# Kernel tuning notes

Hardware: AMD Instinct MI355X
Metric: run time of the kernel (lower is better)

## Reference

```python
import jax, jax.numpy as jnp
import numpy as np

# Ramamoorthi-Hanrahan irradiance matrix constants
C1d, C2d, C3d, C4d, C5d = 0.429043, 0.511664, 0.743125, 0.886227, 0.247708
# Real SH evaluation constants (degree 0..4), standard plenoxels/3DGS values
_SH_C0 = 0.28209479177387814
_SH_C1 = 0.4886025119029199
_SH_C2 = np.array([1.0925484305920792, -1.0925484305920792, 0.31539156525252005, -1.0925484305920792, 0.5462742152960396], np.float32)
_SH_C3 = np.array([-0.5900435899266435, 2.890611442640554, -0.4570457994644658, 0.3731763325901154, -0.4570457994644658, 1.445305721320277, -0.5900435899266435], np.float32)
_SH_C4 = np.array([2.5033429417967046, -1.7701307697799304, 0.9461746957575601, -0.6690465435572892, 0.10578554691520431, -0.6690465435572892, 0.47308734787878004, -1.7701307697799304, 0.6258357354491761], np.float32)
_L = np.array([l for l in range(5) for _ in range(2 * l + 1)], np.float32)  # SH band index per coeff (25,)
_MI = np.array([0, 0, 0, 0, 1, 1, 1, 2, 2, 3])  # triu_indices(4,4)
_MJ = np.array([0, 1, 2, 3, 1, 2, 3, 2, 3, 3])


def safe_normalize(x, eps=1e-20):
    return x * jax.lax.rsqrt(jnp.maximum(jnp.sum(x * x, -1, keepdims=True), eps))


def sh_basis(d):
    # d: (N,3) directions -> (N,25) real SH basis up to degree 4
    x, y, z = d[..., 0], d[..., 1], d[..., 2]
    xx, yy, zz = x * x, y * y, z * z
    xy, yz, xz = x * y, y * z, x * z
    b = [jnp.full_like(x, _SH_C0),
         -_SH_C1 * y, _SH_C1 * z, -_SH_C1 * x,
         _SH_C2[0] * xy, _SH_C2[1] * yz, _SH_C2[2] * (2.0 * zz - xx - yy), _SH_C2[3] * xz, _SH_C2[4] * (xx - yy),
         _SH_C3[0] * y * (3.0 * xx - yy), _SH_C3[1] * xy * z, _SH_C3[2] * y * (4.0 * zz - xx - yy),
         _SH_C3[3] * z * (2.0 * zz - 3.0 * xx - 3.0 * yy), _SH_C3[4] * x * (4.0 * zz - xx - yy),
         _SH_C3[5] * z * (xx - yy), _SH_C3[6] * x * (xx - 3.0 * yy),
         _SH_C4[0] * xy * (xx - yy), _SH_C4[1] * yz * (3.0 * xx - yy), _SH_C4[2] * xy * (7.0 * zz - 1.0),
         _SH_C4[3] * yz * (7.0 * zz - 3.0), _SH_C4[4] * (zz * (35.0 * zz - 30.0) + 3.0),
         _SH_C4[5] * xz * (7.0 * zz - 3.0), _SH_C4[6] * (xx - yy) * (7.0 * zz - 1.0),
         _SH_C4[7] * xz * (xx - yy), _SH_C4[8] * (xx * (xx - 3.0 * yy) - yy * (3.0 * xx - yy))]
    return jnp.stack(b, -1)


def bilinear_lut(lut, uv):
    # lut: (H,W,2); uv: (N,2) in [0,1]; linear filter, clamp boundary (nvdiffrast texel-center convention)
    H, W, _ = lut.shape
    x = uv[:, 0] * W - 0.5
    y = uv[:, 1] * H - 0.5
    x0 = jnp.floor(x); y0 = jnp.floor(y)
    fx = (x - x0)[:, None]; fy = (y - y0)[:, None]
    x0i = jnp.clip(x0.astype(jnp.int32), 0, W - 1); x1i = jnp.clip(x0i + 1, 0, W - 1)
    y0i = jnp.clip(y0.astype(jnp.int32), 0, H - 1); y1i = jnp.clip(y0i + 1, 0, H - 1)
    v00 = lut[y0i, x0i]; v01 = lut[y0i, x1i]; v10 = lut[y1i, x0i]; v11 = lut[y1i, x1i]
    return (v00 * (1.0 - fx) + v01 * fx) * (1.0 - fy) + (v10 * (1.0 - fx) + v11 * fx) * fy


def shade(gb_pos, gb_normal, albedo, ks, kr, km, view_pos, base, fg_lut):
    wo = safe_normalize(view_pos - gb_pos)
    n = gb_normal
    reflvec = safe_normalize(2.0 * jnp.sum(wo * n, -1, keepdims=True) * n - wo)
    # --- diffuse irradiance: n_h^T M n_h per color channel (RH quadratic form) ---
    n_h = jnp.concatenate([n, jnp.ones_like(n[:, :1])], -1)  # (N,4)
    e = base  # (25,3)
    triu = jnp.stack([C1d * e[8], C1d * e[4], C1d * e[7], C2d * e[3], -C1d * e[8],
                      C1d * e[5], C2d * e[1], C3d * e[6], C2d * e[2], C4d * e[0] - C5d * e[6]], 0)  # (10,3)
    M = jnp.zeros((4, 4, 3), base.dtype).at[_MI, _MJ].set(triu).at[_MJ, _MI].set(triu)  # symmetric (4,4,3)
    diffuse_irr = jnp.einsum('ni,ijc,nj->nc', n_h, M, n_h)  # (N,3)
    diffuse = albedo * diffuse_irr
    # --- specular ---
    NdotV = jnp.maximum(jnp.sum(wo * n, -1, keepdims=True), 1e-4)
    fg = bilinear_lut(fg_lut, jnp.concatenate([NdotV, kr], -1))  # (N,2)
    gwk = jnp.exp(-(_L * (_L + 1.0))[None, :] * (kr * kr))  # (N,25) Gauss-Weierstrass kernel per SH band
    spec_irr = gwk[:, :, None] * base[None]  # (N,25,3)
    spec_rad = jnp.einsum('nk,nkc->nc', sh_basis(reflvec), spec_irr)  # (N,3)
    F0 = (1.0 - km) * 0.04 + albedo * km
    reflectance = F0 * fg[:, :1] + fg[:, 1:2]
    spec = spec_rad * reflectance
    rgb = jax.nn.sigmoid(diffuse + spec)
    return rgb, diffuse, spec


def setup_inputs() -> dict:
    key = jax.random.key(0)
    k = jax.random.split(key, 9)
    N = 1048576  # 1024x1024 pixels
    return {
        'gb_pos': jax.random.normal(k[0], (N, 3), jnp.float32),
        'gb_normal': jax.random.normal(k[1], (N, 3), jnp.float32),
        'albedo': jax.random.uniform(k[2], (N, 3), jnp.float32),
        'ks': jax.random.uniform(k[3], (N, 1), jnp.float32),
        'kr': jax.random.uniform(k[4], (N, 1), jnp.float32),
        'km': jax.random.uniform(k[5], (N, 1), jnp.float32),
        'view_pos': jax.random.normal(k[6], (N, 3), jnp.float32),
        'base': jax.random.normal(k[7], (25, 3), jnp.float32) * 0.5,
        'fg_lut': jax.random.uniform(k[8], (256, 256, 2), jnp.float32),
    }


def reference(gb_pos, gb_normal, albedo, ks, kr, km, view_pos, base, fg_lut):
    return shade(gb_pos, gb_normal, albedo, ks, kr, km, view_pos, base, fg_lut)
```

## Files before the change

### kernel.cpp

```cpp
#include <hip/hip_runtime.h>
#include <math.h>


__device__ __forceinline__ void shade_pixel(
    float px, float py, float pz,
    float nx, float ny, float nz,
    float ax, float ay, float az,
    float krv, float kmv,
    float vx, float vy, float vz,
    const float* __restrict__ eb, const float* __restrict__ fg_lut,
    float* rgb, float* dif, float* spc)
{
    float wx = vx - px, wy = vy - py, wz = vz - pz;
    float wl2 = wx*wx + wy*wy + wz*wz;
    float winv = __builtin_amdgcn_rsqf(fmaxf(wl2, 1e-20f));
    wx *= winv; wy *= winv; wz *= winv;

    float ndv = wx*nx + wy*ny + wz*nz;

    float rx = 2.0f*ndv*nx - wx;
    float ry = 2.0f*ndv*ny - wy;
    float rz = 2.0f*ndv*nz - wz;
    float rl2 = rx*rx + ry*ry + rz*rz;
    float rinv = __builtin_amdgcn_rsqf(fmaxf(rl2, 1e-20f));
    rx *= rinv; ry *= rinv; rz *= rinv;

    float NdotV = fmaxf(ndv, 1e-4f);
    float xf = NdotV * 256.0f - 0.5f;
    float yf = krv   * 256.0f - 0.5f;
    float x0f = floorf(xf), y0f = floorf(yf);
    float fx = xf - x0f, fy = yf - y0f;
    int x0i = min(max((int)x0f, 0), 255);
    int x1i = min(x0i + 1, 255);
    int y0i = min(max((int)y0f, 0), 255);
    int y1i = min(y0i + 1, 255);
    const float2* lut2 = (const float2*)fg_lut;
    float2 t00 = lut2[(y0i << 8) + x0i];
    float2 t01 = lut2[(y0i << 8) + x1i];
    float2 t10 = lut2[(y1i << 8) + x0i];
    float2 t11 = lut2[(y1i << 8) + x1i];
    float gxw = 1.0f - fx, gyw = 1.0f - fy;
    float fg0 = (t00.x*gxw + t01.x*fx)*gyw + (t10.x*gxw + t11.x*fx)*fy;
    float fg1 = (t00.y*gxw + t01.y*fx)*gyw + (t10.y*gxw + t11.y*fx)*fy;

    float k2 = krv*krv;
    float g1 = __expf( -2.0f*k2);
    float g2 = __expf( -6.0f*k2);
    float g3 = __expf(-12.0f*k2);
    float g4 = __expf(-20.0f*k2);

    float xx = rx*rx, yy = ry*ry, zz = rz*rz;
    float xy = rx*ry, yz = ry*rz, xz = rx*rz;

    float sr0 = 0.0f, sr1 = 0.0f, sr2 = 0.0f;
#define SHACC(K, EXPR) do { float bk_ = (EXPR);                      \
        sr0 = fmaf(bk_, eb[3*(K)+0], sr0);                           \
        sr1 = fmaf(bk_, eb[3*(K)+1], sr1);                           \
        sr2 = fmaf(bk_, eb[3*(K)+2], sr2); } while (0)

    SHACC(0,  0.28209479177387814f);
    SHACC(1,  (-0.4886025119029199f*ry) * g1);
    SHACC(2,  ( 0.4886025119029199f*rz) * g1);
    SHACC(3,  (-0.4886025119029199f*rx) * g1);
    SHACC(4,  ( 1.0925484305920792f*xy) * g2);
    SHACC(5,  (-1.0925484305920792f*yz) * g2);
    SHACC(6,  ( 0.31539156525252005f*(2.0f*zz - xx - yy)) * g2);
    SHACC(7,  (-1.0925484305920792f*xz) * g2);
    SHACC(8,  ( 0.5462742152960396f*(xx - yy)) * g2);
    SHACC(9,  (-0.5900435899266435f*ry*(3.0f*xx - yy)) * g3);
    SHACC(10, ( 2.890611442640554f*xy*rz) * g3);
    SHACC(11, (-0.4570457994644658f*ry*(4.0f*zz - xx - yy)) * g3);
    SHACC(12, ( 0.3731763325901154f*rz*(2.0f*zz - 3.0f*xx - 3.0f*yy)) * g3);
    SHACC(13, (-0.4570457994644658f*rx*(4.0f*zz - xx - yy)) * g3);
    SHACC(14, ( 1.445305721320277f*rz*(xx - yy)) * g3);
    SHACC(15, (-0.5900435899266435f*rx*(xx - 3.0f*yy)) * g3);
    SHACC(16, ( 2.5033429417967046f*xy*(xx - yy)) * g4);
    SHACC(17, (-1.7701307697799304f*yz*(3.0f*xx - yy)) * g4);
    SHACC(18, ( 0.9461746957575601f*xy*(7.0f*zz - 1.0f)) * g4);
    SHACC(19, (-0.6690465435572892f*yz*(7.0f*zz - 3.0f)) * g4);
    SHACC(20, ( 0.10578554691520431f*(zz*(35.0f*zz - 30.0f) + 3.0f)) * g4);
    SHACC(21, (-0.6690465435572892f*xz*(7.0f*zz - 3.0f)) * g4);
    SHACC(22, ( 0.47308734787878004f*(xx - yy)*(7.0f*zz - 1.0f)) * g4);
    SHACC(23, (-1.7701307697799304f*xz*(xx - yy)) * g4);
    SHACC(24, ( 0.6258357354491761f*(xx*(xx - 3.0f*yy) - yy*(3.0f*xx - yy))) * g4);
#undef SHACC

    float q0  = nx*nx - ny*ny;
    float qz  = nz*nz;
    float qxy = nx*ny, qxz = nx*nz, qyz = ny*nz;

    float alb[3] = {ax, ay, az};
    float srs[3] = {sr0, sr1, sr2};
    #pragma unroll
    for (int c = 0; c < 3; ++c) {
        float e0 = eb[0*3+c], e1 = eb[1*3+c], e2 = eb[2*3+c], e3 = eb[3*3+c],
              e4 = eb[4*3+c], e5 = eb[5*3+c], e6 = eb[6*3+c], e7 = eb[7*3+c],
              e8 = eb[8*3+c];
        float irr = 0.429043f*e8*q0 + 0.743125f*e6*qz + (0.886227f*e0 - 0.247708f*e6)
                  + 2.0f*(0.429043f*(e4*qxy + e7*qxz + e5*qyz)
                        + 0.511664f*(e3*nx + e1*ny + e2*nz));
        float dc = alb[c] * irr;

        float F0 = (1.0f - kmv)*0.04f + alb[c]*kmv;
        float sc = srs[c] * (F0*fg0 + fg1);

        float v = dc + sc;
        rgb[c] = __builtin_amdgcn_rcpf(1.0f + __expf(-v));
        dif[c] = dc;
        spc[c] = sc;
    }
}

__global__ __launch_bounds__(256) void shade_kernel(
    const float* __restrict__ gb_pos, const float* __restrict__ gb_normal,
    const float* __restrict__ albedo, const float* __restrict__ kr,
    const float* __restrict__ km, const float* __restrict__ view_pos,
    const float* __restrict__ base, const float* __restrict__ fg_lut,
    float* __restrict__ out, int N)
{
    int tid = blockIdx.x * blockDim.x + threadIdx.x;
    int p0 = tid * 4;
    if (p0 >= N) return;

    float* out_rgb = out;
    float* out_dif = out + (size_t)3 * N;
    float* out_spc = out + (size_t)6 * N;

    if (p0 + 4 <= N) {
        float P[12], Nr[12], A[12], V[12];
        const float4* pp = (const float4*)gb_pos    + 3*tid;
        const float4* qp = (const float4*)gb_normal + 3*tid;
        const float4* ap = (const float4*)albedo    + 3*tid;
        const float4* vp = (const float4*)view_pos  + 3*tid;
        #pragma unroll
        for (int j = 0; j < 3; ++j) {
            ((float4*)P )[j] = pp[j];
            ((float4*)Nr)[j] = qp[j];
            ((float4*)A )[j] = ap[j];
            ((float4*)V )[j] = vp[j];
        }
        float4 kr4 = ((const float4*)kr)[tid];
        float4 km4 = ((const float4*)km)[tid];
        float krs[4] = {kr4.x, kr4.y, kr4.z, kr4.w};
        float kms[4] = {km4.x, km4.y, km4.z, km4.w};

        float R[12], D[12], S[12];
        #pragma unroll
        for (int j = 0; j < 4; ++j) {
            shade_pixel(P[3*j], P[3*j+1], P[3*j+2],
                        Nr[3*j], Nr[3*j+1], Nr[3*j+2],
                        A[3*j], A[3*j+1], A[3*j+2],
                        krs[j], kms[j],
                        V[3*j], V[3*j+1], V[3*j+2],
                        base, fg_lut,
                        &R[3*j], &D[3*j], &S[3*j]);
        }
        #pragma unroll
        for (int j = 0; j < 3; ++j) {
            ((float4*)out_rgb)[3*tid + j] = ((float4*)R)[j];
            ((float4*)out_dif)[3*tid + j] = ((float4*)D)[j];
            ((float4*)out_spc)[3*tid + j] = ((float4*)S)[j];
        }
    } else {
        for (int p = p0; p < N; ++p) {
            float R[3], D[3], S[3];
            shade_pixel(gb_pos[3*p], gb_pos[3*p+1], gb_pos[3*p+2],
                        gb_normal[3*p], gb_normal[3*p+1], gb_normal[3*p+2],
                        albedo[3*p], albedo[3*p+1], albedo[3*p+2],
                        kr[p], km[p],
                        view_pos[3*p], view_pos[3*p+1], view_pos[3*p+2],
                        base, fg_lut, R, D, S);
            for (int c = 0; c < 3; ++c) {
                out_rgb[3*p+c] = R[c];
                out_dif[3*p+c] = D[c];
                out_spc[3*p+c] = S[c];
            }
        }
    }
}

extern "C" void kernel_launch(void* const* d_in, const int* in_sizes, int n_in,
                              void* d_out, int out_size, void* d_ws, size_t ws_size,
                              hipStream_t stream) {
    const float* gb_pos    = (const float*)d_in[0];
    const float* gb_normal = (const float*)d_in[1];
    const float* albedo    = (const float*)d_in[2];
    const float* kr        = (const float*)d_in[4];
    const float* km        = (const float*)d_in[5];
    const float* view_pos  = (const float*)d_in[6];
    const float* base      = (const float*)d_in[7];
    const float* fg_lut    = (const float*)d_in[8];
    float* out = (float*)d_out;

    int N = in_sizes[0] / 3;
    int nthreads = (N + 3) / 4;
    int block = 256;
    int grid = (nthreads + block - 1) / block;
    shade_kernel<<<grid, block, 0, stream>>>(gb_pos, gb_normal, albedo, kr, km,
                                             view_pos, base, fg_lut, out, N);
}
```

Measured before the change: 128.6 us.

## Stage pixel I/O through LDS with one pixel per thread

```diff
diff --git a/kernel.cpp b/kernel.cpp
--- a/kernel.cpp
+++ b/kernel.cpp
@@ -118,51 +118,57 @@
     const float* __restrict__ base, const float* __restrict__ fg_lut,
     float* __restrict__ out, int N)
 {
-    int tid = blockIdx.x * blockDim.x + threadIdx.x;
-    int p0 = tid * 4;
-    if (p0 >= N) return;
+    __shared__ float s_pos[768], s_nrm[768], s_alb[768], s_view[768];
+    __shared__ float s_kr[256], s_km[256];
+
+    const int t   = threadIdx.x;
+    const int blk = blockIdx.x;
+    const int p0  = blk << 8;
 
     float* out_rgb = out;
     float* out_dif = out + (size_t)3 * N;
     float* out_spc = out + (size_t)6 * N;
 
-    if (p0 + 4 <= N) {
-        float P[12], Nr[12], A[12], V[12];
-        const float4* pp = (const float4*)gb_pos    + 3*tid;
-        const float4* qp = (const float4*)gb_normal + 3*tid;
-        const float4* ap = (const float4*)albedo    + 3*tid;
-        const float4* vp = (const float4*)view_pos  + 3*tid;
-        #pragma unroll
-        for (int j = 0; j < 3; ++j) {
-            ((float4*)P )[j] = pp[j];
-            ((float4*)Nr)[j] = qp[j];
-            ((float4*)A )[j] = ap[j];
-            ((float4*)V )[j] = vp[j];
+    if (p0 + 256 <= N) {
+        if (t < 192) {
+            const size_t b4 = (size_t)blk * 192 + t;
+            ((float4*)s_pos )[t] = ((const float4*)gb_pos   )[b4];
+            ((float4*)s_nrm )[t] = ((const float4*)gb_normal)[b4];
+            ((float4*)s_alb )[t] = ((const float4*)albedo   )[b4];
+            ((float4*)s_view)[t] = ((const float4*)view_pos )[b4];
+        } else {
+            const int u = t - 192;
+            const size_t k4 = (size_t)blk * 64 + u;
+            ((float4*)s_kr)[u] = ((const float4*)kr)[k4];
+            ((float4*)s_km)[u] = ((const float4*)km)[k4];
         }
-        float4 kr4 = ((const float4*)kr)[tid];
-        float4 km4 = ((const float4*)km)[tid];
-        float krs[4] = {kr4.x, kr4.y, kr4.z, kr4.w};
-        float kms[4] = {km4.x, km4.y, km4.z, km4.w};
-
-        float R[12], D[12], S[12];
-        #pragma unroll
-        for (int j = 0; j < 4; ++j) {
-            shade_pixel(P[3*j], P[3*j+1], P[3*j+2],
-                        Nr[3*j], Nr[3*j+1], Nr[3*j+2],
-                        A[3*j], A[3*j+1], A[3*j+2],
-                        krs[j], kms[j],
-                        V[3*j], V[3*j+1], V[3*j+2],
-                        base, fg_lut,
-                        &R[3*j], &D[3*j], &S[3*j]);
-        }
-        #pragma unroll
-        for (int j = 0; j < 3; ++j) {
-            ((float4*)out_rgb)[3*tid + j] = ((float4*)R)[j];
-            ((float4*)out_dif)[3*tid + j] = ((float4*)D)[j];
-            ((float4*)out_spc)[3*tid + j] = ((float4*)S)[j];
+        __syncthreads();
+
+        float px = s_pos[3*t],  py = s_pos[3*t+1],  pz = s_pos[3*t+2];
+        float nx = s_nrm[3*t],  ny = s_nrm[3*t+1],  nz = s_nrm[3*t+2];
+        float ax = s_alb[3*t],  ay = s_alb[3*t+1],  az = s_alb[3*t+2];
+        float vx = s_view[3*t], vy = s_view[3*t+1], vz = s_view[3*t+2];
+        float krv = s_kr[t], kmv = s_km[t];
+        __syncthreads();
+
+        float R[3], D[3], S[3];
+        shade_pixel(px, py, pz, nx, ny, nz, ax, ay, az, krv, kmv,
+                    vx, vy, vz, base, fg_lut, R, D, S);
+
+        s_pos[3*t] = R[0]; s_pos[3*t+1] = R[1]; s_pos[3*t+2] = R[2];
+        s_nrm[3*t] = D[0]; s_nrm[3*t+1] = D[1]; s_nrm[3*t+2] = D[2];
+        s_alb[3*t] = S[0]; s_alb[3*t+1] = S[1]; s_alb[3*t+2] = S[2];
+        __syncthreads();
+
+        if (t < 192) {
+            const size_t b4 = (size_t)blk * 192 + t;
+            ((float4*)out_rgb)[b4] = ((float4*)s_pos)[t];
+            ((float4*)out_dif)[b4] = ((float4*)s_nrm)[t];
+            ((float4*)out_spc)[b4] = ((float4*)s_alb)[t];
         }
     } else {
-        for (int p = p0; p < N; ++p) {
+        const int p = p0 + t;
+        if (p < N) {
             float R[3], D[3], S[3];
             shade_pixel(gb_pos[3*p], gb_pos[3*p+1], gb_pos[3*p+2],
                         gb_normal[3*p], gb_normal[3*p+1], gb_normal[3*p+2],
@@ -193,9 +199,8 @@
     float* out = (float*)d_out;
 
     int N = in_sizes[0] / 3;
-    int nthreads = (N + 3) / 4;
     int block = 256;
-    int grid = (nthreads + block - 1) / block;
+    int grid = (N + block - 1) / block;
     shade_kernel<<<grid, block, 0, stream>>>(gb_pos, gb_normal, albedo, kr, km,
                                              view_pos, base, fg_lut, out, N);
 }
```

After: 123.2 us. 1.04x faster.
